# Optimization experiments

Measured on AMD Instinct MI355X. Metric: run time of the kernel, lower is better.

Reference implementation:

```python
import jax, jax.numpy as jnp
import numpy as np

N1, C, T1, V = 16, 64, 512, 25
NH, DK, DV, BD = 8, 64, 64, 64
DKH, DVH = DK // NH, DV // NH
NB = T1 // BD


def rel_to_abs(x):
    # x: (..., L, 2L-1) -> (..., L, L)  (rel-shift trick)
    *lead, L, _ = x.shape
    x = jnp.pad(x, [(0, 0)] * (x.ndim - 1) + [(0, 1)])      # (..., L, 2L)
    x = x.reshape(*lead, L * 2 * L)
    x = jnp.pad(x, [(0, 0)] * (x.ndim - 1) + [(0, L - 1)])
    x = x.reshape(*lead, L + 1, 2 * L - 1)
    return x[..., :L, L - 1:]


def setup_inputs() -> dict:
    key = jax.random.key(0)
    ks = jax.random.split(key, 6)
    return {
        "x": jax.random.normal(ks[0], (N1, C, T1, V), jnp.float32),
        "w_qkv": jax.random.normal(ks[1], (2 * DK + DV, C), jnp.float32) * 0.05,
        "b_qkv": jax.random.normal(ks[2], (2 * DK + DV,), jnp.float32) * 0.01,
        "w_out": jax.random.normal(ks[3], (DV, DV), jnp.float32) * 0.05,
        "b_out": jax.random.normal(ks[4], (DV,), jnp.float32) * 0.01,
        "key_rel": jax.random.normal(ks[5], (2 * BD - 1, DKH), jnp.float32),
    }


def reference(x, w_qkv, b_qkv, w_out, b_out, key_rel):
    B = N1 * V
    # (N1,C,T1,V) -> (N1*V, C, T1); 1x1 qkv conv == GEMM over channels
    xr = x.transpose(0, 3, 1, 2).reshape(B, C, T1)
    qkv = jnp.einsum('oc,bct->bot', w_qkv, xr) + b_qkv[None, :, None]
    q, k, v = qkv[:, :DK], qkv[:, DK:2 * DK], qkv[:, 2 * DK:]
    # split heads and blocks: (B, NH, dh, NB, BD); all blocks vectorized
    q = q.reshape(B, NH, DKH, NB, BD) * (DKH ** -0.5)
    k = k.reshape(B, NH, DKH, NB, BD)
    v = v.reshape(B, NH, DVH, NB, BD)
    logits = jnp.einsum('bhdnt,bhdns->bhnts', q, k)          # (B,NH,NB,BD,BD)
    # relative position logits (rel-shift)
    qb = q.transpose(0, 1, 3, 4, 2)                          # (B,NH,NB,BD,DKH)
    rel = jnp.einsum('bhntd,md->bhntm', qb, key_rel)         # (B,NH,NB,BD,2BD-1)
    logits = logits + rel_to_abs(rel)
    weights = jax.nn.softmax(logits, axis=-1)
    out = jnp.einsum('bhnts,bhdns->bhdnt', weights, v)       # (B,NH,DVH,NB,BD)
    # combine heads (head-major channels) and blocks along T
    out = out.reshape(B, DV, T1)
    ao = jnp.einsum('oc,bct->bot', w_out, out) + b_out[None, :, None]
    ao = ao.reshape(N1, V, DV, T1).transpose(0, 2, 3, 1)     # (N1,DV,T1,V)
    return jax.nn.relu(ao + x)
```

## Files before the change

### kernel.cpp

```cpp
#include <hip/hip_runtime.h>
#include <math.h>

#define Vc 25
#define QSCALE 0.35355339059327373f

typedef short bf16x8 __attribute__((ext_vector_type(8), may_alias));
typedef short bf16x4 __attribute__((ext_vector_type(4), may_alias));
typedef unsigned int u32a __attribute__((may_alias));
typedef float f32x4 __attribute__((ext_vector_type(4)));

#define FENCE() asm volatile("" ::: "memory")

#define WQA_O 0
#define BQ_O  12288
#define KRT_O 12672
#define WOA_O 13760

__device__ __forceinline__ unsigned short f2bf(float f) {
    unsigned u = __builtin_bit_cast(unsigned, f);
    u = (u + 0x7fff + ((u >> 16) & 1)) >> 16;
    return (unsigned short)u;
}
__device__ __forceinline__ float bf2f(unsigned short h) {
    unsigned u = ((unsigned)h) << 16;
    return __builtin_bit_cast(float, u);
}

__global__ void prep_kernel(const float* __restrict__ w_qkv, const float* __restrict__ b_qkv,
                            const float* __restrict__ w_out, const float* __restrict__ key_rel,
                            unsigned short* __restrict__ ws)
{
    const int gid = blockIdx.x * 256 + threadIdx.x;
    const int gsz = gridDim.x * 256;
    for (int id = gid; id < 12288; id += gsz) {
        int j = id & 7, lane = (id >> 3) & 63, ks = (id >> 9) & 1, mt = id >> 10;
        int m = mt * 16 + (lane & 15);
        int k = ks * 32 + (lane >> 4) * 8 + j;
        ws[WQA_O + id] = f2bf(w_qkv[m * 64 + k] * (m < 64 ? QSCALE : 1.f));
    }
    float* bq = (float*)(ws + BQ_O);
    for (int id = gid; id < 192; id += gsz)
        bq[id] = b_qkv[id] * (id < 64 ? QSCALE : 1.f);
    for (int id = gid; id < 1088; id += gsz) {
        int d = id & 7, m = id >> 3;
        ws[KRT_O + id] = (m < 127) ? f2bf(key_rel[m * 8 + d]) : (unsigned short)0;
    }
    for (int id = gid; id < 4096; id += gsz) {
        int j = id & 7, lane = (id >> 3) & 63, mtg = id >> 9;
        int m = (mtg & 3) * 16 + (lane & 15);
        int k = (mtg >> 2) * 32 + (lane >> 4) * 8 + j;
        ws[WOA_O + id] = f2bf(w_out[m * 64 + k]);
    }
}

#define QT_O   0
#define KT_O   4160
#define VS_O   8320
#define OT_O   12992
#define SCR_O  15552
#define SMEM_U16 21952

__global__ __launch_bounds__(256, 3)
void tcn_attn(const float* __restrict__ x, const float* __restrict__ b_out,
              const unsigned short* __restrict__ ws, float* __restrict__ y)
{
    __shared__ unsigned short sm[SMEM_U16];

    const int tid  = threadIdx.x;
    const int lane = tid & 63;
    const int w    = tid >> 6;
    const int li   = lane & 15;
    const int lq   = lane >> 4;
    const int koff = lq * 8;
    const int n    = blockIdx.x;
    const int b    = blockIdx.y;
    const int n1   = b / Vc;
    const int v    = b - n1 * Vc;
    const int t0   = n * 64;
    const int trow = 16 * w + li;
    const unsigned scr = SCR_O + w * 1600;

    const bf16x8 z8 = {0,0,0,0,0,0,0,0};
    const f32x4  z4 = {0.f,0.f,0.f,0.f};

    for (int i = tid; i < 7776; i += 256)
        ((u32a*)sm)[i] = 0u;

    float xres[16];
    f32x4 pacc[4];
    #pragma unroll
    for (int mt = 0; mt < 4; ++mt)
        #pragma unroll
        for (int r = 0; r < 4; ++r) {
            int o = mt * 16 + lq * 4 + r;
            xres[mt * 4 + r] = x[((n1 * 64 + o) * 512 + t0 + 16 * w + li) * Vc + v];
            pacc[mt][r] = b_out[o];
        }

    #pragma unroll
    for (int i = 0; i < 16; ++i) {
        int e = tid + 256 * i, t = e & 63, c = e >> 6;
        sm[SCR_O + t * 72 + c] = f2bf(x[((n1 * 64 + c) * 512 + t0 + t) * Vc + v]);
    }
    __syncthreads();

    const unsigned short* wq = ws + WQA_O;
    const float* bq = (const float*)(ws + BQ_O);
    #pragma unroll
    for (int sec = 0; sec < 3; ++sec) {
        const int mt = sec * 4 + w;
        bf16x8 a0 = *(const bf16x8*)(wq + ((mt * 2 + 0) * 64 + lane) * 8);
        bf16x8 a1 = *(const bf16x8*)(wq + ((mt * 2 + 1) * 64 + lane) * 8);
        f32x4 acc[4];
        #pragma unroll
        for (int nt = 0; nt < 4; ++nt) {
            #pragma unroll
            for (int r = 0; r < 4; ++r) acc[nt][r] = bq[mt * 16 + lq * 4 + r];
            bf16x8 b0 = *(const bf16x8*)(sm + SCR_O + (16 * nt + li) * 72 + koff);
            bf16x8 b1 = *(const bf16x8*)(sm + SCR_O + (16 * nt + li) * 72 + 32 + koff);
            acc[nt] = __builtin_amdgcn_mfma_f32_16x16x32_bf16(a0, b0, acc[nt], 0, 0, 0);
            acc[nt] = __builtin_amdgcn_mfma_f32_16x16x32_bf16(a1, b1, acc[nt], 0, 0, 0);
        }
        const int h2 = 2 * w + (lq >> 1);
        if (sec < 2) {
            const unsigned base = (sec == 0 ? QT_O : KT_O) + h2 * 520 + (lq & 1) * 4;
            #pragma unroll
            for (int nt = 0; nt < 4; ++nt) {
                bf16x4 p;
                p.x = (short)f2bf(acc[nt][0]);
                p.y = (short)f2bf(acc[nt][1]);
                p.z = (short)f2bf(acc[nt][2]);
                p.w = (short)f2bf(acc[nt][3]);
                *(bf16x4*)(sm + base + (16 * nt + li) * 8) = p;
            }
        } else {
            #pragma unroll
            for (int nt = 0; nt < 4; ++nt)
                #pragma unroll
                for (int r = 0; r < 4; ++r)
                    sm[VS_O + h2 * 584 + ((lq & 1) * 4 + r) * 72 + 16 * nt + li] = f2bf(acc[nt][r]);
        }
    }
    __syncthreads();

    bf16x8 br[5];
    #pragma unroll
    for (int j = 0; j < 5; ++j)
        br[j] = *(const bf16x8*)(ws + KRT_O + (16 * (3 - w + j) + li) * 8 + koff);

    for (int h = 0; h < 8; ++h) {
        bf16x8 aq = *(const bf16x8*)(sm + QT_O + h * 520 + trow * 8 + koff);
        if (lane >= 16) aq = z8;

        f32x4 qk[4];
        #pragma unroll
        for (int nt = 0; nt < 4; ++nt) {
            bf16x8 bk = *(const bf16x8*)(sm + KT_O + h * 520 + (16 * nt + li) * 8 + koff);
            qk[nt] = __builtin_amdgcn_mfma_f32_16x16x32_bf16(aq, bk, z4, 0, 0, 0);
        }
        #pragma unroll
        for (int j = 0; j < 5; ++j) {
            f32x4 rl = __builtin_amdgcn_mfma_f32_16x16x32_bf16(aq, br[j], z4, 0, 0, 0);
            bf16x4 p;
            p.x = (short)f2bf(rl[0]);
            p.y = (short)f2bf(rl[1]);
            p.z = (short)f2bf(rl[2]);
            p.w = (short)f2bf(rl[3]);
            *(bf16x4*)(sm + scr + (16 * j + li) * 20 + 4 * lq) = p;
        }
        FENCE();
        float ex[4][4], lsum[4] = {0.f, 0.f, 0.f, 0.f};
        #pragma unroll
        for (int nt = 0; nt < 4; ++nt)
            #pragma unroll
            for (int r = 0; r < 4; ++r) {
                int mp = 16 * nt + li - 4 * lq - r + 15;
                float rv = bf2f(sm[scr + mp * 20 + 4 * lq + r]);
                float e = __expf(qk[nt][r] + rv);
                ex[nt][r] = e;
                lsum[r] += e;
            }
        FENCE();
        float linv[4];
        #pragma unroll
        for (int r = 0; r < 4; ++r) {
            float s = lsum[r];
            s += __shfl_xor(s, 1);
            s += __shfl_xor(s, 2);
            s += __shfl_xor(s, 4);
            s += __shfl_xor(s, 8);
            linv[r] = 1.0f / s;
        }
        #pragma unroll
        for (int nt = 0; nt < 4; ++nt)
            #pragma unroll
            for (int r = 0; r < 4; ++r)
                sm[scr + (4 * lq + r) * 72 + 16 * nt + li] = f2bf(ex[nt][r] * linv[r]);
        FENCE();
        f32x4 av = z4;
        #pragma unroll
        for (int ks = 0; ks < 2; ++ks) {
            bf16x8 aa = *(const bf16x8*)(sm + scr + li * 72 + ks * 32 + koff);
            bf16x8 bv = *(const bf16x8*)(sm + VS_O + h * 584 + (li & 7) * 72 + ks * 32 + koff);
            av = __builtin_amdgcn_mfma_f32_16x16x32_bf16(aa, bv, av, 0, 0, 0);
        }
        if (li < 8) {
            #pragma unroll
            for (int r = 0; r < 4; ++r)
                sm[OT_O + (16 * w + 4 * lq + r) * 40 + (h & 3) * 8 + li] = f2bf(av[r]);
        }
        if ((h & 3) == 3) {
            FENCE();
            bf16x8 bo = *(const bf16x8*)(sm + OT_O + trow * 40 + koff);
            const int g = h >> 2;
            #pragma unroll
            for (int mt = 0; mt < 4; ++mt) {
                bf16x8 ao = *(const bf16x8*)(ws + WOA_O + ((g * 4 + mt) * 64 + lane) * 8);
                pacc[mt] = __builtin_amdgcn_mfma_f32_16x16x32_bf16(ao, bo, pacc[mt], 0, 0, 0);
            }
        }
        FENCE();
    }

    #pragma unroll
    for (int mt = 0; mt < 4; ++mt)
        #pragma unroll
        for (int r = 0; r < 4; ++r) {
            int o = mt * 16 + lq * 4 + r;
            int idx = ((n1 * 64 + o) * 512 + t0 + 16 * w + li) * Vc + v;
            y[idx] = fmaxf(pacc[mt][r] + xres[mt * 4 + r], 0.f);
        }
}

extern "C" void kernel_launch(void* const* d_in, const int* in_sizes, int n_in,
                              void* d_out, int out_size, void* d_ws, size_t ws_size,
                              hipStream_t stream) {
    const float* x       = (const float*)d_in[0];
    const float* w_qkv   = (const float*)d_in[1];
    const float* b_qkv   = (const float*)d_in[2];
    const float* w_out   = (const float*)d_in[3];
    const float* b_out   = (const float*)d_in[4];
    const float* key_rel = (const float*)d_in[5];
    float* y = (float*)d_out;
    unsigned short* ws = (unsigned short*)d_ws;

    prep_kernel<<<dim3(96), dim3(256), 0, stream>>>(w_qkv, b_qkv, w_out, key_rel, ws);
    dim3 grid(512 / 64, 400);
    tcn_attn<<<grid, dim3(256), 0, stream>>>(x, b_out, ws, y);
}
```

Before: 239.7 us.

## Drop prep kernel, software-pipeline head loop, DPP row sums, defer softmax normalize

Removes the separate weight-prep kernel launch: each block now loads fp32 weights, key_rel and w_out straight from global memory and converts them to bf16 in registers. The per-head loop is fully unrolled and software-pipelined, so the QK and relative-logit MFMAs for the next head are issued while the current head's softmax runs. Row sums use DPP adds instead of shuffles, and the 1/sum normalization moves after the PV MFMA, so it scales the small output rather than every probability. In exchange there is redundant per-block conversion work, more global loads of w_out, and higher register pressure from holding two heads' MFMA results under the 3-blocks-per-SM launch bound.

```diff
diff --git a/kernel.cpp b/kernel.cpp
--- a/kernel.cpp
+++ b/kernel.cpp
@@ -8,13 +8,9 @@
 typedef short bf16x4 __attribute__((ext_vector_type(4), may_alias));
 typedef unsigned int u32a __attribute__((may_alias));
 typedef float f32x4 __attribute__((ext_vector_type(4)));
+typedef float f32x4a __attribute__((ext_vector_type(4), may_alias));
 
 #define FENCE() asm volatile("" ::: "memory")
-
-#define WQA_O 0
-#define BQ_O  12288
-#define KRT_O 12672
-#define WOA_O 13760
 
 __device__ __forceinline__ unsigned short f2bf(float f) {
     unsigned u = __builtin_bit_cast(unsigned, f);
@@ -26,31 +22,18 @@
     return __builtin_bit_cast(float, u);
 }
 
-__global__ void prep_kernel(const float* __restrict__ w_qkv, const float* __restrict__ b_qkv,
-                            const float* __restrict__ w_out, const float* __restrict__ key_rel,
-                            unsigned short* __restrict__ ws)
-{
-    const int gid = blockIdx.x * 256 + threadIdx.x;
-    const int gsz = gridDim.x * 256;
-    for (int id = gid; id < 12288; id += gsz) {
-        int j = id & 7, lane = (id >> 3) & 63, ks = (id >> 9) & 1, mt = id >> 10;
-        int m = mt * 16 + (lane & 15);
-        int k = ks * 32 + (lane >> 4) * 8 + j;
-        ws[WQA_O + id] = f2bf(w_qkv[m * 64 + k] * (m < 64 ? QSCALE : 1.f));
-    }
-    float* bq = (float*)(ws + BQ_O);
-    for (int id = gid; id < 192; id += gsz)
-        bq[id] = b_qkv[id] * (id < 64 ? QSCALE : 1.f);
-    for (int id = gid; id < 1088; id += gsz) {
-        int d = id & 7, m = id >> 3;
-        ws[KRT_O + id] = (m < 127) ? f2bf(key_rel[m * 8 + d]) : (unsigned short)0;
-    }
-    for (int id = gid; id < 4096; id += gsz) {
-        int j = id & 7, lane = (id >> 3) & 63, mtg = id >> 9;
-        int m = (mtg & 3) * 16 + (lane & 15);
-        int k = (mtg >> 2) * 32 + (lane >> 4) * 8 + j;
-        ws[WOA_O + id] = f2bf(w_out[m * 64 + k]);
-    }
+template<int CTRL>
+__device__ __forceinline__ float dpp_add(float x) {
+    int xi = __builtin_bit_cast(int, x);
+    int yi = __builtin_amdgcn_update_dpp(0, xi, CTRL, 0xf, 0xf, true);
+    return x + __builtin_bit_cast(float, yi);
+}
+__device__ __forceinline__ float row_sum16(float s) {
+    s = dpp_add<0xB1>(s);
+    s = dpp_add<0x4E>(s);
+    s = dpp_add<0x141>(s);
+    s = dpp_add<0x140>(s);
+    return s;
 }
 
 #define QT_O   0
@@ -61,8 +44,10 @@
 #define SMEM_U16 21952
 
 __global__ __launch_bounds__(256, 3)
-void tcn_attn(const float* __restrict__ x, const float* __restrict__ b_out,
-              const unsigned short* __restrict__ ws, float* __restrict__ y)
+void tcn_attn(const float* __restrict__ x, const float* __restrict__ w_qkv,
+              const float* __restrict__ b_qkv, const float* __restrict__ w_out,
+              const float* __restrict__ b_out, const float* __restrict__ key_rel,
+              float* __restrict__ y)
 {
     __shared__ unsigned short sm[SMEM_U16];
 
@@ -104,18 +89,31 @@
     }
     __syncthreads();
 
-    const unsigned short* wq = ws + WQA_O;
-    const float* bq = (const float*)(ws + BQ_O);
     #pragma unroll
     for (int sec = 0; sec < 3; ++sec) {
         const int mt = sec * 4 + w;
-        bf16x8 a0 = *(const bf16x8*)(wq + ((mt * 2 + 0) * 64 + lane) * 8);
-        bf16x8 a1 = *(const bf16x8*)(wq + ((mt * 2 + 1) * 64 + lane) * 8);
+        const int m  = mt * 16 + li;
+        const float wscale = (sec == 0) ? QSCALE : 1.0f;
+        bf16x8 a0, a1;
+        {
+            const float* p0 = w_qkv + m * 64 + koff;
+            const float* p1 = w_qkv + m * 64 + 32 + koff;
+            f32x4a v00 = *(const f32x4a*)p0, v01 = *(const f32x4a*)(p0 + 4);
+            f32x4a v10 = *(const f32x4a*)p1, v11 = *(const f32x4a*)(p1 + 4);
+            #pragma unroll
+            for (int j = 0; j < 4; ++j) {
+                a0[j]     = (short)f2bf(v00[j] * wscale);
+                a0[4 + j] = (short)f2bf(v01[j] * wscale);
+                a1[j]     = (short)f2bf(v10[j] * wscale);
+                a1[4 + j] = (short)f2bf(v11[j] * wscale);
+            }
+        }
         f32x4 acc[4];
         #pragma unroll
         for (int nt = 0; nt < 4; ++nt) {
             #pragma unroll
-            for (int r = 0; r < 4; ++r) acc[nt][r] = bq[mt * 16 + lq * 4 + r];
+            for (int r = 0; r < 4; ++r)
+                acc[nt][r] = b_qkv[mt * 16 + lq * 4 + r] * wscale;
             bf16x8 b0 = *(const bf16x8*)(sm + SCR_O + (16 * nt + li) * 72 + koff);
             bf16x8 b1 = *(const bf16x8*)(sm + SCR_O + (16 * nt + li) * 72 + 32 + koff);
             acc[nt] = __builtin_amdgcn_mfma_f32_16x16x32_bf16(a0, b0, acc[nt], 0, 0, 0);
@@ -145,28 +143,67 @@
 
     bf16x8 br[5];
     #pragma unroll
-    for (int j = 0; j < 5; ++j)
-        br[j] = *(const bf16x8*)(ws + KRT_O + (16 * (3 - w + j) + li) * 8 + koff);
-
-    for (int h = 0; h < 8; ++h) {
+    for (int j = 0; j < 5; ++j) {
+        int base = (16 * (3 - w + j) + li) * 8 + koff;
+        if (base + 7 <= 1015) {
+            f32x4a v0 = *(const f32x4a*)(key_rel + base);
+            f32x4a v1 = *(const f32x4a*)(key_rel + base + 4);
+            #pragma unroll
+            for (int jj = 0; jj < 4; ++jj) {
+                br[j][jj]     = (short)f2bf(v0[jj]);
+                br[j][4 + jj] = (short)f2bf(v1[jj]);
+            }
+        } else {
+            #pragma unroll
+            for (int jj = 0; jj < 8; ++jj) {
+                int idx = base + jj; if (idx > 1015) idx = 1015;
+                br[j][jj] = (short)f2bf(key_rel[idx]);
+            }
+        }
+    }
+
+    auto FRONT = [&](int h, f32x4* qk, f32x4* rl) {
         bf16x8 aq = *(const bf16x8*)(sm + QT_O + h * 520 + trow * 8 + koff);
         if (lane >= 16) aq = z8;
-
-        f32x4 qk[4];
         #pragma unroll
         for (int nt = 0; nt < 4; ++nt) {
             bf16x8 bk = *(const bf16x8*)(sm + KT_O + h * 520 + (16 * nt + li) * 8 + koff);
             qk[nt] = __builtin_amdgcn_mfma_f32_16x16x32_bf16(aq, bk, z4, 0, 0, 0);
         }
         #pragma unroll
+        for (int j = 0; j < 5; ++j)
+            rl[j] = __builtin_amdgcn_mfma_f32_16x16x32_bf16(aq, br[j], z4, 0, 0, 0);
+    };
+
+    f32x4 qk[4], rl[5];
+    FRONT(0, qk, rl);
+
+    #pragma unroll
+    for (int h = 0; h < 8; ++h) {
+        #pragma unroll
         for (int j = 0; j < 5; ++j) {
-            f32x4 rl = __builtin_amdgcn_mfma_f32_16x16x32_bf16(aq, br[j], z4, 0, 0, 0);
             bf16x4 p;
-            p.x = (short)f2bf(rl[0]);
-            p.y = (short)f2bf(rl[1]);
-            p.z = (short)f2bf(rl[2]);
-            p.w = (short)f2bf(rl[3]);
+            p.x = (short)f2bf(rl[j][0]);
+            p.y = (short)f2bf(rl[j][1]);
+            p.z = (short)f2bf(rl[j][2]);
+            p.w = (short)f2bf(rl[j][3]);
             *(bf16x4*)(sm + scr + (16 * j + li) * 20 + 4 * lq) = p;
+        }
+        f32x4 qkn[4], rln[5];
+        if (h < 7) FRONT(h + 1, qkn, rln);
+        bf16x8 ao[4];
+        if ((h & 3) == 3) {
+            const int g = h >> 2;
+            #pragma unroll
+            for (int mt = 0; mt < 4; ++mt) {
+                const float* p0 = w_out + (mt * 16 + li) * 64 + g * 32 + koff;
+                f32x4a v0 = *(const f32x4a*)p0, v1 = *(const f32x4a*)(p0 + 4);
+                #pragma unroll
+                for (int jj = 0; jj < 4; ++jj) {
+                    ao[mt][jj]     = (short)f2bf(v0[jj]);
+                    ao[mt][4 + jj] = (short)f2bf(v1[jj]);
+                }
+            }
         }
         FENCE();
         float ex[4][4], lsum[4] = {0.f, 0.f, 0.f, 0.f};
@@ -183,19 +220,13 @@
         FENCE();
         float linv[4];
         #pragma unroll
-        for (int r = 0; r < 4; ++r) {
-            float s = lsum[r];
-            s += __shfl_xor(s, 1);
-            s += __shfl_xor(s, 2);
-            s += __shfl_xor(s, 4);
-            s += __shfl_xor(s, 8);
-            linv[r] = 1.0f / s;
-        }
+        for (int r = 0; r < 4; ++r)
+            linv[r] = 1.0f / row_sum16(lsum[r]);
         #pragma unroll
         for (int nt = 0; nt < 4; ++nt)
             #pragma unroll
             for (int r = 0; r < 4; ++r)
-                sm[scr + (4 * lq + r) * 72 + 16 * nt + li] = f2bf(ex[nt][r] * linv[r]);
+                sm[scr + (4 * lq + r) * 72 + 16 * nt + li] = f2bf(ex[nt][r]);
         FENCE();
         f32x4 av = z4;
         #pragma unroll
@@ -207,19 +238,22 @@
         if (li < 8) {
             #pragma unroll
             for (int r = 0; r < 4; ++r)
-                sm[OT_O + (16 * w + 4 * lq + r) * 40 + (h & 3) * 8 + li] = f2bf(av[r]);
+                sm[OT_O + (16 * w + 4 * lq + r) * 40 + (h & 3) * 8 + li] = f2bf(av[r] * linv[r]);
         }
         if ((h & 3) == 3) {
             FENCE();
             bf16x8 bo = *(const bf16x8*)(sm + OT_O + trow * 40 + koff);
-            const int g = h >> 2;
-            #pragma unroll
-            for (int mt = 0; mt < 4; ++mt) {
-                bf16x8 ao = *(const bf16x8*)(ws + WOA_O + ((g * 4 + mt) * 64 + lane) * 8);
-                pacc[mt] = __builtin_amdgcn_mfma_f32_16x16x32_bf16(ao, bo, pacc[mt], 0, 0, 0);
-            }
-        }
-        FENCE();
+            #pragma unroll
+            for (int mt = 0; mt < 4; ++mt)
+                pacc[mt] = __builtin_amdgcn_mfma_f32_16x16x32_bf16(ao[mt], bo, pacc[mt], 0, 0, 0);
+        }
+        FENCE();
+        if (h < 7) {
+            #pragma unroll
+            for (int i = 0; i < 4; ++i) qk[i] = qkn[i];
+            #pragma unroll
+            for (int j = 0; j < 5; ++j) rl[j] = rln[j];
+        }
     }
 
     #pragma unroll
@@ -242,9 +276,7 @@
     const float* b_out   = (const float*)d_in[4];
     const float* key_rel = (const float*)d_in[5];
     float* y = (float*)d_out;
-    unsigned short* ws = (unsigned short*)d_ws;
-
-    prep_kernel<<<dim3(96), dim3(256), 0, stream>>>(w_qkv, b_qkv, w_out, key_rel, ws);
+
     dim3 grid(512 / 64, 400);
-    tcn_attn<<<grid, dim3(256), 0, stream>>>(x, b_out, ws, y);
-}
+    tcn_attn<<<grid, dim3(256), 0, stream>>>(x, w_qkv, b_qkv, w_out, b_out, key_rel, y);
+}
```

New measurement: 256.5 us. +7.0%, slower.
